# Optimization experiments

Hardware: AMD Instinct MI355X
Metric: run time of the kernel (lower is better)

## Reference

```python
import jax, jax.numpy as jnp
import numpy as np

SPECIAL = 4  # special_word_num

def _lstm_cell(x, h, c, Wih, Whh, b):
    # torch gate order: i, f, g, o ; gates = x@Wih.T + h@Whh.T + b
    g = x @ Wih.T + h @ Whh.T + b
    i, f, gg, o = jnp.split(g, 4, axis=-1)
    c_new = jax.nn.sigmoid(f) * c + jax.nn.sigmoid(i) * jnp.tanh(gg)
    h_new = jax.nn.sigmoid(o) * jnp.tanh(c_new)
    return h_new, c_new

def _lstm_scan(xs, h0, c0, Wih, Whh, b):
    def step(carry, x):
        h, c = carry
        h, c = _lstm_cell(x, h, c, Wih, Whh, b)
        return (h, c), h
    (hT, cT), hs = jax.lax.scan(step, (h0, c0), xs)
    return hs, hT, cT  # hs: [T, B, H]

def _forward(article, art_lens, tar_len, emb, enc_Wih_f, enc_Whh_f, enc_b_f,
             enc_Wih_b, enc_Whh_b, enc_b_b, init_enc_h, init_enc_c,
             dec_hW, dec_cW, attn_wm, attn_wq, proj_W1, proj_b1, proj_W2,
             dec_Wih, dec_Whh, dec_b):
    Tsrc, B, _ = article.shape
    H = init_enc_h.shape[1]
    # ---- encoder: 1-layer bidirectional LSTM with learned init states ----
    h0f = jnp.broadcast_to(init_enc_h[0], (B, H)); c0f = jnp.broadcast_to(init_enc_c[0], (B, H))
    h0b = jnp.broadcast_to(init_enc_h[1], (B, H)); c0b = jnp.broadcast_to(init_enc_c[1], (B, H))
    out_f, hTf, cTf = _lstm_scan(article, h0f, c0f, enc_Wih_f, enc_Whh_f, enc_b_f)
    out_b, hTb, cTb = _lstm_scan(article[::-1], h0b, c0b, enc_Wih_b, enc_Whh_b, enc_b_b)
    enc_art = jnp.concatenate([out_f, out_b[::-1]], axis=-1)  # [T, B, 2H]
    final_h = jnp.concatenate([hTf, hTb], axis=-1)  # [B, 2H]
    final_c = jnp.concatenate([cTf, cTb], axis=-1)
    init_h = final_h @ dec_hW  # [B, H]
    init_c = final_c @ dec_cW
    # ---- attention memory + mask ----
    attention = jnp.einsum('tbe,eh->bth', enc_art, attn_wm)  # [B, T, H]
    mask = jnp.arange(Tsrc)[None, :] < art_lens[:, None]      # [B, T]
    lens = art_lens.astype(attention.dtype)[:, None]
    seq_mean = jnp.sum(attention * mask[:, :, None], axis=1) / lens  # [B, H]
    def project(x):
        return jnp.tanh(x @ proj_W1 + proj_b1) @ proj_W2
    init_out = project(jnp.concatenate([init_h, seq_mean], axis=1))  # [B, H/2]
    # ---- sequential decoder over tar_len steps (lax.scan) ----
    embs = emb[SPECIAL + jnp.arange(tar_len)]  # [Ttgt, E]
    NEG = jnp.asarray(-1e9, attention.dtype)
    def dec_step(carry, emb_i):
        h, c, prev_out = carry
        x = jnp.concatenate([jnp.broadcast_to(emb_i, (B, emb_i.shape[0])), prev_out], axis=1)
        h, c = _lstm_cell(x, h, c, dec_Wih, dec_Whh, dec_b)
        query = h @ attn_wq                                   # [B, H]
        score = jnp.einsum('bh,bth->bt', query, attention)
        probs = jax.nn.softmax(jnp.where(mask, score, NEG), axis=-1)
        context = jnp.einsum('bt,bth->bh', probs, attention)
        dec_out = project(jnp.concatenate([h, context], axis=1))
        return (h, c, dec_out), (dec_out, h, c)
    _, (dec_all, h_all, c_all) = jax.lax.scan(dec_step, (init_h, init_c, init_out), embs)
    # stack(dim=0).transpose(0,1) -> batch-first
    return (dec_all.transpose(1, 0, 2), h_all.transpose(1, 0, 2), c_all.transpose(1, 0, 2))

def setup_inputs() -> dict:
    key = jax.random.key(0)
    ks = jax.random.split(key, 20)
    B, Tsrc, Ttgt = 32, 1024, 64
    H, E, V = 512, 256, 50000  # n_hidden, emb_dim/2, vocab
    EMB_DIM, ENC_OUT, OUT = 2 * E, 2 * H, H // 2
    def n(k, shape, s=0.05):
        return (jax.random.normal(k, shape, jnp.float32) * s).astype(jnp.float32)
    return {
        'article': n(ks[0], (Tsrc, B, EMB_DIM), 1.0),
        'art_lens': jnp.full((B,), Tsrc, jnp.int32),
        'tar_len': Ttgt,
        'emb': n(ks[1], (V, E)),
        'enc_Wih_f': n(ks[2], (4 * H, EMB_DIM)), 'enc_Whh_f': n(ks[3], (4 * H, H)), 'enc_b_f': n(ks[4], (4 * H,)),
        'enc_Wih_b': n(ks[5], (4 * H, EMB_DIM)), 'enc_Whh_b': n(ks[6], (4 * H, H)), 'enc_b_b': n(ks[7], (4 * H,)),
        'init_enc_h': n(ks[8], (2, H), 0.01), 'init_enc_c': n(ks[9], (2, H), 0.01),
        'dec_hW': n(ks[10], (ENC_OUT, H)), 'dec_cW': n(ks[11], (ENC_OUT, H)),
        'attn_wm': n(ks[12], (ENC_OUT, H)), 'attn_wq': n(ks[13], (H, H)),
        'proj_W1': n(ks[14], (2 * H, H)), 'proj_b1': n(ks[15], (H,)), 'proj_W2': n(ks[16], (H, OUT)),
        'dec_Wih': n(ks[17], (4 * H, H)), 'dec_Whh': n(ks[18], (4 * H, H)), 'dec_b': n(ks[19], (4 * H,)),
    }

def reference(article, art_lens, tar_len, emb, enc_Wih_f, enc_Whh_f, enc_b_f,
              enc_Wih_b, enc_Whh_b, enc_b_b, init_enc_h, init_enc_c,
              dec_hW, dec_cW, attn_wm, attn_wq, proj_W1, proj_b1, proj_W2,
              dec_Wih, dec_Whh, dec_b):
    return _forward(article, art_lens, tar_len, emb, enc_Wih_f, enc_Whh_f, enc_b_f,
                    enc_Wih_b, enc_Whh_b, enc_b_b, init_enc_h, init_enc_c,
                    dec_hW, dec_cW, attn_wm, attn_wq, proj_W1, proj_b1, proj_W2,
                    dec_Wih, dec_Whh, dec_b)
```

## Files before the change

kernel.cpp:

```cpp
#include <hip/hip_runtime.h>


#define DI __device__ __forceinline__

constexpr int BATCH = 32;
constexpr int TS = 1024;
constexpr int TG = 64;
constexpr int HID = 512;
constexpr int GD = 2048;
constexpr int EDIM = 256;
constexpr int SPECIAL = 4;
constexpr size_t OFF_H = (size_t)BATCH * TG * EDIM;
constexpr size_t OFF_C = OFF_H + (size_t)BATCH * TG * HID;
constexpr int FLAG_STRIDE = 16;

typedef __attribute__((ext_vector_type(8))) short bf16x8;
typedef __attribute__((ext_vector_type(4))) float f32x4;

DI float b2f(unsigned short u) {
  union { unsigned int i; float f; } v; v.i = ((unsigned int)u) << 16; return v.f;
}
DI unsigned short f2b(float f) {
  union { float f; unsigned int i; } v; v.f = f;
  unsigned int r = v.i + 0x7fffu + ((v.i >> 16) & 1u);
  return (unsigned short)(r >> 16);
}
DI float sigm(float x) { return 1.0f / (1.0f + expf(-x)); }
DI float ldf(const void* p, size_t i, int f32f) {
  return f32f ? ((const float*)p)[i] : b2f(((const unsigned short*)p)[i]);
}
DI void stf(void* p, size_t i, float v, int f32f) {
  if (f32f) ((float*)p)[i] = v; else ((unsigned short*)p)[i] = f2b(v);
}
DI unsigned int ald(const unsigned int* p) {
  return __hip_atomic_load(p, __ATOMIC_RELAXED, __HIP_MEMORY_SCOPE_AGENT);
}
DI float aldf(const float* p) {
  return __hip_atomic_load(p, __ATOMIC_RELAXED, __HIP_MEMORY_SCOPE_AGENT);
}
DI void ast(unsigned int* p, unsigned int v) {
  __hip_atomic_store(p, v, __ATOMIC_RELAXED, __HIP_MEMORY_SCOPE_AGENT);
}
DI void astf(float* p, float v) {
  __hip_atomic_store(p, v, __ATOMIC_RELAXED, __HIP_MEMORY_SCOPE_AGENT);
}

__global__ void detect_k(const void* art, int* flag) {
  int tid = threadIdx.x;
  float x = ((const float*)art)[tid + 1024];
  float a = fabsf(x);
  int sane = (x == 0.0f) || (a > 1e-8f && a < 1e4f);
  unsigned long long m = __ballot(sane);
  __shared__ int cnt[4];
  if ((tid & 63) == 0) cnt[tid >> 6] = __popcll(m);
  __syncthreads();
  if (tid == 0) flag[0] = (cnt[0] + cnt[1] + cnt[2] + cnt[3] > 128) ? 1 : 0;
}

__global__ void fill_sig_k(unsigned short* o, int n) {
  int g = blockIdx.x * 256 + threadIdx.x;
  if (g < n) o[g] = 0x42F6;
}

__global__ void pack_gate_k(const void* __restrict__ W,
                            unsigned short* __restrict__ pk, const int* dtf) {
  int f32f = dtf[0];
  int g = blockIdx.x * 256 + threadIdx.x;
  if (g >= (GD * HID) / 8) return;
  int lane = g & 63;
  int kk = (g >> 6) & 15;
  int tile = g >> 10;
  int p = tile * 16 + (lane & 15);
  int nloc = p & 63, blk = p >> 6;
  int orow = (nloc >> 4) * HID + blk * 16 + (nloc & 15);
  int k = kk * 32 + (lane >> 4) * 8;
  unsigned short tmp[8];
#pragma unroll
  for (int j = 0; j < 8; ++j) tmp[j] = f2b(ldf(W, (size_t)orow * HID + k + j, f32f));
  *(uint4*)(pk + (size_t)g * 8) = *(uint4*)tmp;
}

__global__ void pack_wm_k(const void* __restrict__ wm,
                          unsigned short* __restrict__ pk, const int* dtf) {
  int f32f = dtf[0];
  int g = blockIdx.x * 256 + threadIdx.x;
  if (g >= 32 * 32 * 64) return;
  int lane = g & 63;
  int kk = (g >> 6) & 31;
  int nt = g >> 11;
  int col = nt * 16 + (lane & 15);
  int kb = kk * 32 + (lane >> 4) * 8;
  unsigned short tmp[8];
#pragma unroll
  for (int j = 0; j < 8; ++j) tmp[j] = f2b(ldf(wm, (size_t)(kb + j) * HID + col, f32f));
  *(uint4*)(pk + (size_t)g * 8) = *(uint4*)tmp;
}

__global__ void pack_bn_k(const void* __restrict__ W, unsigned short* __restrict__ pk,
                          int K, int N, int total, const int* dtf) {
  int f32f = dtf[0];
  int g = blockIdx.x * 256 + threadIdx.x;
  if (g >= total) return;
  int lane = g & 63;
  int KK = K >> 5;
  int t = g >> 6;
  int kk = t % KK;
  int nt = t / KK;
  int col = nt * 16 + (lane & 15);
  int kb = kk * 32 + (lane >> 4) * 8;
  unsigned short tmp[8];
#pragma unroll
  for (int j = 0; j < 8; ++j) tmp[j] = f2b(ldf(W, (size_t)(kb + j) * N + col, f32f));
  *(uint4*)(pk + (size_t)g * 8) = *(uint4*)tmp;
}

__global__ void pack_bf16_k(const void* __restrict__ src,
                            unsigned short* __restrict__ dst, int n, const int* dtf) {
  int f32f = dtf[0];
  int g = blockIdx.x * 256 + threadIdx.x;
  if (g < n) dst[g] = f2b(ldf(src, g, f32f));
}

__global__ __launch_bounds__(256, 1) void enc_all_k(
    const unsigned short* __restrict__ artb,
    unsigned short* __restrict__ outF, unsigned short* __restrict__ outB,
    const unsigned short* __restrict__ hIF, const unsigned short* __restrict__ hIB,
    float* __restrict__ cF, float* __restrict__ cB,
    const unsigned short* __restrict__ pkXF, const unsigned short* __restrict__ pkHF,
    const unsigned short* __restrict__ pkXB, const unsigned short* __restrict__ pkHB,
    const void* __restrict__ bF, const void* __restrict__ bB,
    int* __restrict__ bar, const int* dtf) {
  const int f32f = dtf[0];
  const int blk = blockIdx.x;
  const int dir = blk >> 5;
  const int blk16 = blk & 31;
  const int tid = threadIdx.x;
  const int lane = tid & 63;
  const int wv = tid >> 6;
  const int tile = blk16 * 4 + wv;

  __shared__ unsigned short lstage[BATCH * HID];
  __shared__ float gbuf[BATCH * 68];

  const unsigned short* pkX = dir ? pkXB : pkXF;
  const unsigned short* pkH = dir ? pkHB : pkHF;
  const void* bias = dir ? bB : bF;
  unsigned short* out = dir ? outB : outF;
  const unsigned short* hI = dir ? hIB : hIF;
  float* cg = dir ? cB : cF;
  int* flp = bar + dir * 32 * FLAG_STRIDE;

  bf16x8 wx[16], wh[16];
  {
    const unsigned short* px = pkX + ((size_t)tile * 16 * 64 + lane) * 8;
    const unsigned short* ph = pkH + ((size_t)tile * 16 * 64 + lane) * 8;
#pragma unroll
    for (int kk = 0; kk < 16; ++kk) {
      wx[kk] = *(const bf16x8*)(px + (size_t)kk * 64 * 8);
      wh[kk] = *(const bf16x8*)(ph + (size_t)kk * 64 * 8);
    }
  }
  const int gb = tid >> 3;
  const int gj = (tid & 7) * 2;
  float c0 = cg[gb * HID + blk16 * 16 + gj];
  float c1 = cg[gb * HID + blk16 * 16 + gj + 1];

  const int r0 = lane & 15;
  const int r1 = 16 + r0;
  const int kbb = (lane >> 4) * 8;
  const int nloc = wv * 16 + (lane & 15);
  const int orow = (nloc >> 4) * HID + blk16 * 16 + (nloc & 15);
  const float bv = ldf(bias, orow, f32f);

  f32x4 acc0 = {0.f, 0.f, 0.f, 0.f};
  f32x4 acc1 = {0.f, 0.f, 0.f, 0.f};

  {
    const int ts0 = dir ? (TS - 1) : 0;
#pragma unroll
    for (int it = 0; it < 8; ++it) {
      int ci = it * 256 + tid;
      int row = ci >> 6;
      int k8 = (ci & 63) << 3;
      uint4 v = *(const uint4*)(artb + (size_t)ts0 * BATCH * HID +
                                (size_t)row * HID + k8);
      unsigned off = (unsigned)(row * 1024 + ((k8 * 2) ^ ((row & 7) << 4)));
      *(uint4*)((char*)lstage + off) = v;
    }
    __syncthreads();
#pragma unroll
    for (int kk = 0; kk < 16; ++kk) {
      unsigned o0 = (unsigned)(r0 * 1024 + (((kk * 32 + kbb) * 2) ^ ((r0 & 7) << 4)));
      unsigned o1 = (unsigned)(r1 * 1024 + (((kk * 32 + kbb) * 2) ^ ((r0 & 7) << 4)));
      bf16x8 a0 = *(const bf16x8*)((const char*)lstage + o0);
      bf16x8 a1 = *(const bf16x8*)((const char*)lstage + o1);
      acc0 = __builtin_amdgcn_mfma_f32_16x16x32_bf16(a0, wx[kk], acc0, 0, 0, 0);
      acc1 = __builtin_amdgcn_mfma_f32_16x16x32_bf16(a1, wx[kk], acc1, 0, 0, 0);
    }
  }

  for (int t = 0; t < TS; ++t) {
    const int tsrc = dir ? (TS - 1 - t) : t;
    if (t > 0) {
      if (wv == 0) {
        const int target = t;
        for (;;) {
          int v = (lane < 32)
              ? __hip_atomic_load(flp + lane * FLAG_STRIDE, __ATOMIC_RELAXED,
                                  __HIP_MEMORY_SCOPE_AGENT)
              : 0x7fffffff;
          if (__all(v >= target)) break;
          __builtin_amdgcn_s_sleep(2);
        }
      }
      __syncthreads();
    }
    unsigned int* hu = (t == 0)
        ? (unsigned int*)hI
        : (unsigned int*)(out + (size_t)(tsrc + (dir ? 1 : -1)) * BATCH * HID);
    unsigned int hreg[32];
#pragma unroll
    for (int it = 0; it < 32; ++it) hreg[it] = ald(hu + it * 256 + tid);
    __syncthreads();
#pragma unroll
    for (int it = 0; it < 32; ++it) {
      int dw = it * 256 + tid;
      int row = dw >> 8;
      unsigned lb = (unsigned)(row * 1024 +
                               (((dw & 252) << 2) ^ ((row & 7) << 4)) +
                               ((dw & 3) << 2));
      *(unsigned int*)((char*)lstage + lb) = hreg[it];
    }
    __syncthreads();
#pragma unroll
    for (int kk = 0; kk < 16; ++kk) {
      unsigned o0 = (unsigned)(r0 * 1024 + (((kk * 32 + kbb) * 2) ^ ((r0 & 7) << 4)));
      unsigned o1 = (unsigned)(r1 * 1024 + (((kk * 32 + kbb) * 2) ^ ((r0 & 7) << 4)));
      bf16x8 a0 = *(const bf16x8*)((const char*)lstage + o0);
      bf16x8 a1 = *(const bf16x8*)((const char*)lstage + o1);
      acc0 = __builtin_amdgcn_mfma_f32_16x16x32_bf16(a0, wh[kk], acc0, 0, 0, 0);
      acc1 = __builtin_amdgcn_mfma_f32_16x16x32_bf16(a1, wh[kk], acc1, 0, 0, 0);
    }
#pragma unroll
    for (int r = 0; r < 4; ++r) {
      int brow = (lane >> 4) * 4 + r;
      gbuf[brow * 68 + nloc] = acc0[r] + bv;
      gbuf[(16 + brow) * 68 + nloc] = acc1[r] + bv;
    }
    __syncthreads();
    {
      float gi0 = gbuf[gb * 68 + gj],      gf0 = gbuf[gb * 68 + 16 + gj];
      float gg0 = gbuf[gb * 68 + 32 + gj], go0 = gbuf[gb * 68 + 48 + gj];
      float gi1 = gbuf[gb * 68 + gj + 1],      gf1 = gbuf[gb * 68 + 16 + gj + 1];
      float gg1 = gbuf[gb * 68 + 32 + gj + 1], go1 = gbuf[gb * 68 + 48 + gj + 1];
      float cn0 = sigm(gf0) * c0 + sigm(gi0) * tanhf(gg0); c0 = cn0;
      float cn1 = sigm(gf1) * c1 + sigm(gi1) * tanhf(gg1); c1 = cn1;
      unsigned int hv = (unsigned int)f2b(sigm(go0) * tanhf(cn0)) |
                        ((unsigned int)f2b(sigm(go1) * tanhf(cn1)) << 16);
      ast((unsigned int*)out + (size_t)tsrc * (BATCH * HID / 2) +
              gb * (HID / 2) + blk16 * 8 + (tid & 7), hv);
    }
    if (t + 1 < TS) {
      __syncthreads();
      if (wv == 0 && lane == 0)
        __hip_atomic_store(flp + blk16 * FLAG_STRIDE, t + 1,
                           __ATOMIC_RELAXED, __HIP_MEMORY_SCOPE_AGENT);
      const int tn = dir ? (TS - 2 - t) : (t + 1);
#pragma unroll
      for (int it = 0; it < 8; ++it) {
        int ci = it * 256 + tid;
        int row = ci >> 6;
        int k8 = (ci & 63) << 3;
        uint4 v = *(const uint4*)(artb + (size_t)tn * BATCH * HID +
                                  (size_t)row * HID + k8);
        unsigned off = (unsigned)(row * 1024 + ((k8 * 2) ^ ((row & 7) << 4)));
        *(uint4*)((char*)lstage + off) = v;
      }
      __syncthreads();
      acc0 = (f32x4){0.f, 0.f, 0.f, 0.f};
      acc1 = (f32x4){0.f, 0.f, 0.f, 0.f};
#pragma unroll
      for (int kk = 0; kk < 16; ++kk) {
        unsigned o0 = (unsigned)(r0 * 1024 + (((kk * 32 + kbb) * 2) ^ ((r0 & 7) << 4)));
        unsigned o1 = (unsigned)(r1 * 1024 + (((kk * 32 + kbb) * 2) ^ ((r0 & 7) << 4)));
        bf16x8 a0 = *(const bf16x8*)((const char*)lstage + o0);
        bf16x8 a1 = *(const bf16x8*)((const char*)lstage + o1);
        acc0 = __builtin_amdgcn_mfma_f32_16x16x32_bf16(a0, wx[kk], acc0, 0, 0, 0);
        acc1 = __builtin_amdgcn_mfma_f32_16x16x32_bf16(a1, wx[kk], acc1, 0, 0, 0);
      }
    }
  }
  cg[gb * HID + blk16 * 16 + gj] = c0;
  cg[gb * HID + blk16 * 16 + gj + 1] = c1;
}

__global__ __launch_bounds__(512, 1) void dec_all_k(
    unsigned short* __restrict__ xdec,
    unsigned short* __restrict__ hd0, unsigned short* __restrict__ hd1,
    const float* __restrict__ cdec,
    const unsigned short* __restrict__ pkX, const unsigned short* __restrict__ pkH,
    const void* __restrict__ dbias,
    const unsigned short* __restrict__ att,
    const unsigned short* __restrict__ pkq,
    const unsigned short* __restrict__ pkw1,
    const unsigned short* __restrict__ b1p,
    const unsigned short* __restrict__ pkw2,
    const void* __restrict__ emb, const int* __restrict__ lens,
    void* __restrict__ dout,
    float* __restrict__ qg,
    unsigned int* __restrict__ ctxb,
    float* __restrict__ zg,
    int* __restrict__ flags, const int* dtf) {
  const int f32f = dtf[0];
  const int blk = blockIdx.x;
  const int tid = threadIdx.x;
  const int lane = tid & 63;
  const int wv = tid >> 6;
  __shared__ __align__(16) char smem[49152];

  const int gb = tid >> 3;
  const int gj = (tid & 7) * 2;
  const int r0 = lane & 15;
  const int r1 = 16 + r0;
  const int kbb = (lane >> 4) * 8;
  const int nloc = wv * 16 + (lane & 15);
  float c0 = 0.f, c1 = 0.f, bv = 0.f;
  bf16x8 cwx[16], cwh[16];
  if (tid < 256) {
    c0 = cdec[gb * HID + blk * 16 + gj];
    c1 = cdec[gb * HID + blk * 16 + gj + 1];
    int orow = (nloc >> 4) * HID + blk * 16 + (nloc & 15);
    bv = ldf(dbias, orow, f32f);
    const int tile = blk * 4 + wv;
    const unsigned short* px = pkX + ((size_t)tile * 16 * 64 + lane) * 8;
    const unsigned short* ph = pkH + ((size_t)tile * 16 * 64 + lane) * 8;
#pragma unroll
    for (int kk = 0; kk < 16; ++kk) {
      cwx[kk] = *(const bf16x8*)(px + (size_t)kk * 64 * 8);
      cwh[kk] = *(const bf16x8*)(ph + (size_t)kk * 64 * 8);
    }
  }

  int ep = 0;
  auto gbar = [&]() {
    __syncthreads();
    ++ep;
    if (wv == 0) {
      if (lane == 0)
        __hip_atomic_store(flags + blk * FLAG_STRIDE, ep, __ATOMIC_RELAXED,
                           __HIP_MEMORY_SCOPE_AGENT);
      for (;;) {
        int v = (lane < 32)
            ? __hip_atomic_load(flags + lane * FLAG_STRIDE, __ATOMIC_RELAXED,
                                __HIP_MEMORY_SCOPE_AGENT)
            : 0x7fffffff;
        if (__all(v >= ep)) break;
        __builtin_amdgcn_s_sleep(2);
      }
    }
    __syncthreads();
  };

  auto stage8k = [&](const unsigned int* src, unsigned short* lstage) {
    unsigned int rg[16];
#pragma unroll
    for (int it = 0; it < 16; ++it) rg[it] = ald(src + it * 512 + tid);
#pragma unroll
    for (int it = 0; it < 16; ++it) {
      int dw = it * 512 + tid;
      int row = dw >> 8;
      unsigned lb = (unsigned)(row * 1024 +
                               (((dw & 252) << 2) ^ ((row & 7) << 4)) +
                               ((dw & 3) << 2));
      *(unsigned int*)((char*)lstage + lb) = rg[it];
    }
  };

  auto afrag = [&](const unsigned short* lstage, int kk, bf16x8& a0, bf16x8& a1) {
    unsigned o0 = (unsigned)(r0 * 1024 + (((kk * 32 + kbb) * 2) ^ ((r0 & 7) << 4)));
    unsigned o1 = (unsigned)(r1 * 1024 + (((kk * 32 + kbb) * 2) ^ ((r0 & 7) << 4)));
    a0 = *(const bf16x8*)((const char*)lstage + o0);
    a1 = *(const bf16x8*)((const char*)lstage + o1);
  };

  for (int i = 0; i < TG; ++i) {
    unsigned short* hin = (i & 1) ? hd1 : hd0;
    unsigned short* hout = (i & 1) ? hd0 : hd1;
    f32x4 zacc0 = {0.f, 0.f, 0.f, 0.f};
    f32x4 zacc1 = {0.f, 0.f, 0.f, 0.f};

    {
      unsigned short* lstage = (unsigned short*)smem;
      float* gbuf = (float*)(smem + 32768);
      f32x4 acc0 = {0.f, 0.f, 0.f, 0.f};
      f32x4 acc1 = {0.f, 0.f, 0.f, 0.f};
      unsigned int hreg[32];
      if (tid < 256) {
        const unsigned int* xu = (const unsigned int*)xdec;
        unsigned int xreg[32];
#pragma unroll
        for (int it = 0; it < 32; ++it) xreg[it] = ald(xu + it * 256 + tid);
#pragma unroll
        for (int it = 0; it < 32; ++it) {
          int dw = it * 256 + tid;
          int row = dw >> 8;
          unsigned lb = (unsigned)(row * 1024 +
                                   (((dw & 252) << 2) ^ ((row & 7) << 4)) +
                                   ((dw & 3) << 2));
          *(unsigned int*)((char*)lstage + lb) = xreg[it];
        }
      }
      __syncthreads();
      if (tid < 256) {
        const unsigned int* hu = (const unsigned int*)hin;
#pragma unroll
        for (int it = 0; it < 32; ++it) hreg[it] = ald(hu + it * 256 + tid);
#pragma unroll
        for (int kk = 0; kk < 16; ++kk) {
          bf16x8 a0, a1;
          afrag(lstage, kk, a0, a1);
          acc0 = __builtin_amdgcn_mfma_f32_16x16x32_bf16(a0, cwx[kk], acc0, 0, 0, 0);
          acc1 = __builtin_amdgcn_mfma_f32_16x16x32_bf16(a1, cwx[kk], acc1, 0, 0, 0);
        }
      }
      __syncthreads();
      if (tid < 256) {
#pragma unroll
        for (int it = 0; it < 32; ++it) {
          int dw = it * 256 + tid;
          int row = dw >> 8;
          unsigned lb = (unsigned)(row * 1024 +
                                   (((dw & 252) << 2) ^ ((row & 7) << 4)) +
                                   ((dw & 3) << 2));
          *(unsigned int*)((char*)lstage + lb) = hreg[it];
        }
      }
      __syncthreads();
      if (tid < 256) {
#pragma unroll
        for (int kk = 0; kk < 16; ++kk) {
          bf16x8 a0, a1;
          afrag(lstage, kk, a0, a1);
          acc0 = __builtin_amdgcn_mfma_f32_16x16x32_bf16(a0, cwh[kk], acc0, 0, 0, 0);
          acc1 = __builtin_amdgcn_mfma_f32_16x16x32_bf16(a1, cwh[kk], acc1, 0, 0, 0);
        }
#pragma unroll
        for (int r = 0; r < 4; ++r) {
          int brow = (lane >> 4) * 4 + r;
          gbuf[brow * 68 + nloc] = acc0[r] + bv;
          gbuf[(16 + brow) * 68 + nloc] = acc1[r] + bv;
        }
      }
      __syncthreads();
      if (tid < 256) {
        float gi0 = gbuf[gb * 68 + gj],      gf0 = gbuf[gb * 68 + 16 + gj];
        float gg0 = gbuf[gb * 68 + 32 + gj], go0 = gbuf[gb * 68 + 48 + gj];
        float gi1 = gbuf[gb * 68 + gj + 1],      gf1 = gbuf[gb * 68 + 16 + gj + 1];
        float gg1 = gbuf[gb * 68 + 32 + gj + 1], go1 = gbuf[gb * 68 + 48 + gj + 1];
        float cn0 = sigm(gf0) * c0 + sigm(gi0) * tanhf(gg0); c0 = cn0;
        float cn1 = sigm(gf1) * c1 + sigm(gi1) * tanhf(gg1); c1 = cn1;
        float hn0 = sigm(go0) * tanhf(cn0);
        float hn1 = sigm(go1) * tanhf(cn1);
        ast((unsigned int*)hout + gb * (HID / 2) + blk * 8 + (tid & 7),
            (unsigned int)f2b(hn0) | ((unsigned int)f2b(hn1) << 16));
        size_t e0 = ((size_t)gb * TG + i) * HID + blk * 16 + gj;
        stf(dout, OFF_H + e0, hn0, f32f);
        stf(dout, OFF_H + e0 + 1, hn1, f32f);
        stf(dout, OFF_C + e0, cn0, f32f);
        stf(dout, OFF_C + e0 + 1, cn1, f32f);
      }
    }
    gbar();

    {
      unsigned short* lstage = (unsigned short*)smem;
      float* part = (float*)(smem + 32768);
      stage8k((const unsigned int*)hout, lstage);
      __syncthreads();
      f32x4 acc0 = {0.f, 0.f, 0.f, 0.f};
      f32x4 acc1 = {0.f, 0.f, 0.f, 0.f};
#pragma unroll
      for (int j = 0; j < 2; ++j) {
        int kk = wv * 2 + j;
        bf16x8 a0, a1;
        afrag(lstage, kk, a0, a1);
        bf16x8 bq = *(const bf16x8*)(pkq + ((size_t)(blk * 16 + kk) * 64 + lane) * 8);
        acc0 = __builtin_amdgcn_mfma_f32_16x16x32_bf16(a0, bq, acc0, 0, 0, 0);
        acc1 = __builtin_amdgcn_mfma_f32_16x16x32_bf16(a1, bq, acc1, 0, 0, 0);
        bf16x8 bw = *(const bf16x8*)(pkw1 + ((size_t)(blk * 32 + kk) * 64 + lane) * 8);
        zacc0 = __builtin_amdgcn_mfma_f32_16x16x32_bf16(a0, bw, zacc0, 0, 0, 0);
        zacc1 = __builtin_amdgcn_mfma_f32_16x16x32_bf16(a1, bw, zacc1, 0, 0, 0);
      }
#pragma unroll
      for (int r = 0; r < 4; ++r) {
        int m0 = (lane >> 4) * 4 + r;
        part[wv * 512 + m0 * 16 + (lane & 15)] = acc0[r];
        part[wv * 512 + (m0 + 16) * 16 + (lane & 15)] = acc1[r];
      }
      __syncthreads();
      {
        float s = 0.f;
#pragma unroll
        for (int w = 0; w < 8; ++w) s += part[w * 512 + tid];
        int bb2 = tid >> 4, cl = tid & 15;
        astf(qg + (size_t)bb2 * HID + blk * 16 + cl, s);
      }
    }
    gbar();

    {
      const int b = blk;
      const int len = lens[b];
      float* cred = (float*)smem;
      float* mwl  = (float*)(smem + 16384);
      float* lwl  = (float*)(smem + 16448);
      float* qf   = (float*)(smem + 16512);
      float* ctxf = (float*)(smem + 18560);
      qf[tid] = aldf(qg + (size_t)b * HID + tid);
      __syncthreads();
      float qv[8];
#pragma unroll
      for (int e = 0; e < 8; ++e) qv[e] = qf[lane * 8 + e];
      float m = -1e30f, l = 0.f;
      float ca[8] = {0.f, 0.f, 0.f, 0.f, 0.f, 0.f, 0.f, 0.f};
      const unsigned short* ab = att + ((size_t)b * TS + wv * 128) * HID + lane * 8;
      for (int tt = 0; tt < 128; tt += 4) {
        int t = wv * 128 + tt;
        bf16x8 rr0 = *(const bf16x8*)(ab + (size_t)(tt + 0) * HID);
        bf16x8 rr1 = *(const bf16x8*)(ab + (size_t)(tt + 1) * HID);
        bf16x8 rr2 = *(const bf16x8*)(ab + (size_t)(tt + 2) * HID);
        bf16x8 rr3 = *(const bf16x8*)(ab + (size_t)(tt + 3) * HID);
        float s0 = 0.f, s1 = 0.f, s2 = 0.f, s3 = 0.f;
#pragma unroll
        for (int e = 0; e < 8; ++e) {
          float q = qv[e];
          s0 += q * b2f(((const unsigned short*)&rr0)[e]);
          s1 += q * b2f(((const unsigned short*)&rr1)[e]);
          s2 += q * b2f(((const unsigned short*)&rr2)[e]);
          s3 += q * b2f(((const unsigned short*)&rr3)[e]);
        }
        for (int o = 32; o; o >>= 1) {
          s0 += __shfl_xor(s0, o, 64); s1 += __shfl_xor(s1, o, 64);
          s2 += __shfl_xor(s2, o, 64); s3 += __shfl_xor(s3, o, 64);
        }
        bool v0 = (t < len), v1 = (t + 1 < len), v2 = (t + 2 < len), v3 = (t + 3 < len);
        float smax = fmaxf(fmaxf(v0 ? s0 : -1e30f, v1 ? s1 : -1e30f),
                           fmaxf(v2 ? s2 : -1e30f, v3 ? s3 : -1e30f));
        if (smax > m) {
          float sc2 = expf(m - smax);
          l *= sc2;
#pragma unroll
          for (int e = 0; e < 8; ++e) ca[e] *= sc2;
          m = smax;
        }
        if (v0) { float p = expf(s0 - m); l += p;
#pragma unroll
          for (int e = 0; e < 8; ++e) ca[e] += p * b2f(((const unsigned short*)&rr0)[e]); }
        if (v1) { float p = expf(s1 - m); l += p;
#pragma unroll
          for (int e = 0; e < 8; ++e) ca[e] += p * b2f(((const unsigned short*)&rr1)[e]); }
        if (v2) { float p = expf(s2 - m); l += p;
#pragma unroll
          for (int e = 0; e < 8; ++e) ca[e] += p * b2f(((const unsigned short*)&rr2)[e]); }
        if (v3) { float p = expf(s3 - m); l += p;
#pragma unroll
          for (int e = 0; e < 8; ++e) ca[e] += p * b2f(((const unsigned short*)&rr3)[e]); }
      }
#pragma unroll
      for (int e = 0; e < 8; ++e) cred[wv * 512 + lane * 8 + e] = ca[e];
      if (lane == 0) { mwl[wv] = m; lwl[wv] = l; }
      __syncthreads();
      {
        float M = -1e30f;
#pragma unroll
        for (int w = 0; w < 8; ++w) M = fmaxf(M, mwl[w]);
        float L = 0.f, s = 0.f;
#pragma unroll
        for (int w = 0; w < 8; ++w) {
          float sc2 = expf(mwl[w] - M);
          L += lwl[w] * sc2;
          s += cred[w * 512 + tid] * sc2;
        }
        ctxf[tid] = s / L;
      }
      __syncthreads();
      if (tid < 256) {
        unsigned int d = (unsigned int)f2b(ctxf[2 * tid]) |
                         ((unsigned int)f2b(ctxf[2 * tid + 1]) << 16);
        ast(ctxb + b * 256 + tid, d);
      }
    }
    gbar();

    {
      unsigned short* lstage = (unsigned short*)smem;
      float* part = (float*)(smem + 32768);
      stage8k(ctxb, lstage);
      __syncthreads();
#pragma unroll
      for (int j = 0; j < 2; ++j) {
        int kkl = wv * 2 + j;
        bf16x8 a0, a1;
        afrag(lstage, kkl, a0, a1);
        bf16x8 bb = *(const bf16x8*)(pkw1 + ((size_t)(blk * 32 + 16 + kkl) * 64 + lane) * 8);
        zacc0 = __builtin_amdgcn_mfma_f32_16x16x32_bf16(a0, bb, zacc0, 0, 0, 0);
        zacc1 = __builtin_amdgcn_mfma_f32_16x16x32_bf16(a1, bb, zacc1, 0, 0, 0);
      }
#pragma unroll
      for (int r = 0; r < 4; ++r) {
        int m0 = (lane >> 4) * 4 + r;
        part[wv * 512 + m0 * 16 + (lane & 15)] = zacc0[r];
        part[wv * 512 + (m0 + 16) * 16 + (lane & 15)] = zacc1[r];
      }
      __syncthreads();
      {
        float s = 0.f;
#pragma unroll
        for (int w = 0; w < 8; ++w) s += part[w * 512 + tid];
        int bb2 = tid >> 4, cl = tid & 15;
        int col = blk * 16 + cl;
        astf(zg + (size_t)bb2 * HID + col, tanhf(b2f(b1p[col]) + s));
      }
    }
    gbar();

    {
      unsigned short* lstage = (unsigned short*)smem;
      float* part = (float*)(smem + 32768);
      if (blk < 16) {
        unsigned int rg[16];
#pragma unroll
        for (int it = 0; it < 16; ++it) {
          int dw = it * 512 + tid;
          int b = dw >> 8, cp = dw & 255;
          float z0 = aldf(zg + (size_t)b * HID + 2 * cp);
          float z1 = aldf(zg + (size_t)b * HID + 2 * cp + 1);
          rg[it] = (unsigned int)f2b(z0) | ((unsigned int)f2b(z1) << 16);
        }
#pragma unroll
        for (int it = 0; it < 16; ++it) {
          int dw = it * 512 + tid;
          int row = dw >> 8;
          unsigned lb = (unsigned)(row * 1024 +
                                   (((dw & 252) << 2) ^ ((row & 7) << 4)) +
                                   ((dw & 3) << 2));
          *(unsigned int*)((char*)lstage + lb) = rg[it];
        }
      }
      __syncthreads();
      f32x4 acc0 = {0.f, 0.f, 0.f, 0.f};
      f32x4 acc1 = {0.f, 0.f, 0.f, 0.f};
      if (blk < 16) {
#pragma unroll
        for (int j = 0; j < 2; ++j) {
          int kk = wv * 2 + j;
          bf16x8 a0, a1;
          afrag(lstage, kk, a0, a1);
          bf16x8 bb = *(const bf16x8*)(pkw2 + ((size_t)(blk * 16 + kk) * 64 + lane) * 8);
          acc0 = __builtin_amdgcn_mfma_f32_16x16x32_bf16(a0, bb, acc0, 0, 0, 0);
          acc1 = __builtin_amdgcn_mfma_f32_16x16x32_bf16(a1, bb, acc1, 0, 0, 0);
        }
#pragma unroll
        for (int r = 0; r < 4; ++r) {
          int m0 = (lane >> 4) * 4 + r;
          part[wv * 512 + m0 * 16 + (lane & 15)] = acc0[r];
          part[wv * 512 + (m0 + 16) * 16 + (lane & 15)] = acc1[r];
        }
      }
      __syncthreads();
      if (blk < 16) {
        float s = 0.f;
#pragma unroll
        for (int w = 0; w < 8; ++w) s += part[w * 512 + tid];
        int bb2 = tid >> 4, cl = tid & 15;
        int col = blk * 16 + cl;
        stf(dout, ((size_t)bb2 * TG + i) * EDIM + col, s, f32f);
        unsigned short xb = f2b(s);
        int ob = __shfl_xor((int)xb, 1);
        if (!(tid & 1))
          ast((unsigned int*)xdec + bb2 * 256 + 128 + (col >> 1),
              (unsigned int)xb | ((unsigned int)(ob & 0xffff) << 16));
      }
      if (blk == 16) {
#pragma unroll
        for (int it = 0; it < 8; ++it) {
          int idx = it * 512 + tid;
          int b = idx >> 7, np = idx & 127;
          float e0 = ldf(emb, (size_t)(SPECIAL + i + 1) * EDIM + 2 * np, f32f);
          float e1 = ldf(emb, (size_t)(SPECIAL + i + 1) * EDIM + 2 * np + 1, f32f);
          ast((unsigned int*)xdec + b * 256 + np,
              (unsigned int)f2b(e0) | ((unsigned int)f2b(e1) << 16));
        }
      }
    }
    gbar();
  }
}

__global__ __launch_bounds__(256) void attn_mm_k(
    const unsigned short* __restrict__ outF, const unsigned short* __restrict__ outB,
    const unsigned short* __restrict__ pkwm, unsigned short* __restrict__ att) {
  __shared__ char ldsA[4 * 1040];
  int bid = blockIdx.x;
  int bn = bid & 7, bm = bid >> 3;
  int tid = threadIdx.x, lane = tid & 63, wv = tid >> 6;
  int r0 = bm * 64;
  f32x4 acc[2][2] = {};
  int srow = tid >> 2, skb = tid & 3;
  int mt0 = (wv & 1) * 2, nt0 = (wv >> 1) * 2;
  for (int kk = 0; kk < 32; ++kk) {
    int kg = kk * 32 + skb * 8;
    const unsigned short* src = (kg < HID)
        ? (outF + (size_t)(r0 + srow) * HID + kg)
        : (outB + (size_t)(r0 + srow) * HID + (kg - HID));
    uint4 v = *(const uint4*)src;
    __syncthreads();
    *(uint4*)(ldsA + skb * 1040 + srow * 16) = v;
    __syncthreads();
    bf16x8 a[2], bb[2];
#pragma unroll
    for (int mi = 0; mi < 2; ++mi) {
      int rl = (mt0 + mi) * 16 + (lane & 15);
      a[mi] = *(const bf16x8*)(ldsA + (lane >> 4) * 1040 + rl * 16);
    }
#pragma unroll
    for (int nj = 0; nj < 2; ++nj) {
      int ntg = bn * 4 + nt0 + nj;
      bb[nj] = *(const bf16x8*)(pkwm + ((size_t)(ntg * 32 + kk) * 64 + lane) * 8);
    }
#pragma unroll
    for (int mi = 0; mi < 2; ++mi)
#pragma unroll
      for (int nj = 0; nj < 2; ++nj)
        acc[mi][nj] = __builtin_amdgcn_mfma_f32_16x16x32_bf16(a[mi], bb[nj], acc[mi][nj], 0, 0, 0);
  }
#pragma unroll
  for (int mi = 0; mi < 2; ++mi)
#pragma unroll
    for (int nj = 0; nj < 2; ++nj)
#pragma unroll
      for (int r = 0; r < 4; ++r) {
        int row = r0 + (mt0 + mi) * 16 + (lane >> 4) * 4 + r;
        int t = row >> 5, b = row & 31;
        int h = bn * 64 + (nt0 + nj) * 16 + (lane & 15);
        att[((size_t)b * TS + t) * HID + h] = f2b(acc[mi][nj][r]);
      }
}

__global__ void init_states_k(const void* __restrict__ ih, const void* __restrict__ ic,
                              unsigned short* hIF, unsigned short* hIB,
                              float* cF, float* cB, int* bar, const int* dtf) {
  int f32f = dtf[0];
  int g = blockIdx.x * 256 + threadIdx.x;
  if (g < (64 + 32) * FLAG_STRIDE)
    __hip_atomic_store(bar + g, 0, __ATOMIC_RELAXED, __HIP_MEMORY_SCOPE_AGENT);
  int b = g >> 9, j = g & 511;
  hIF[b * HID + j] = f2b(ldf(ih, j, f32f));
  hIB[b * HID + j] = f2b(ldf(ih, HID + j, f32f));
  cF[b * HID + j] = ldf(ic, j, f32f);
  cB[b * HID + j] = ldf(ic, HID + j, f32f);
}

__global__ void seqmean_k(const unsigned short* __restrict__ att,
                          const int* __restrict__ lens, float* __restrict__ sm) {
  int b = blockIdx.x, tid = threadIdx.x;
  int len = lens[b];
  float a0 = 0.f, a1 = 0.f;
  for (int t = 0; t < len; ++t) {
    const unsigned short* row = att + ((size_t)b * TS + t) * HID;
    a0 += b2f(row[tid]);
    a1 += b2f(row[tid + 256]);
  }
  float fl = (float)len;
  sm[b * HID + tid] = a0 / fl;
  sm[b * HID + tid + 256] = a1 / fl;
}

__global__ void mv_bb_k(const unsigned short* __restrict__ A1,
                        const unsigned short* __restrict__ A2,
                        const void* __restrict__ W, unsigned short* __restrict__ o,
                        const int* dtf) {
  int f32f = dtf[0];
  int g = blockIdx.x * 256 + threadIdx.x;
  int b = g >> 9, n = g & 511;
  float acc = 0.f;
  for (int k = 0; k < HID; ++k) acc += b2f(A1[b * HID + k]) * ldf(W, (size_t)k * HID + n, f32f);
  for (int k = 0; k < HID; ++k) acc += b2f(A2[b * HID + k]) * ldf(W, (size_t)(HID + k) * HID + n, f32f);
  o[b * HID + n] = f2b(acc);
}

__global__ void mv_ff_k(const float* __restrict__ A1, const float* __restrict__ A2,
                        const void* __restrict__ W, float* __restrict__ o, const int* dtf) {
  int f32f = dtf[0];
  int g = blockIdx.x * 256 + threadIdx.x;
  int b = g >> 9, n = g & 511;
  float acc = 0.f;
  for (int k = 0; k < HID; ++k) acc += A1[b * HID + k] * ldf(W, (size_t)k * HID + n, f32f);
  for (int k = 0; k < HID; ++k) acc += A2[b * HID + k] * ldf(W, (size_t)(HID + k) * HID + n, f32f);
  o[b * HID + n] = acc;
}

__global__ void proj1_k(const unsigned short* __restrict__ A1, const float* __restrict__ A2,
                        const void* __restrict__ W1p, const void* __restrict__ b1p,
                        unsigned short* __restrict__ z, const int* dtf) {
  int f32f = dtf[0];
  int g = blockIdx.x * 256 + threadIdx.x;
  int b = g >> 9, n = g & 511;
  float acc = ldf(b1p, n, f32f);
  for (int k = 0; k < HID; ++k) acc += b2f(A1[b * HID + k]) * ldf(W1p, (size_t)k * HID + n, f32f);
  for (int k = 0; k < HID; ++k) acc += A2[b * HID + k] * ldf(W1p, (size_t)(HID + k) * HID + n, f32f);
  z[b * HID + n] = f2b(tanhf(acc));
}

__global__ void proj2_init_k(const unsigned short* __restrict__ z,
                             const void* __restrict__ W2, const void* __restrict__ emb,
                             unsigned short* __restrict__ xdec, const int* dtf) {
  int f32f = dtf[0];
  int g = blockIdx.x * 256 + threadIdx.x;
  int b = g >> 8, n = g & 255;
  float acc = 0.f;
  for (int k = 0; k < HID; ++k) acc += b2f(z[b * HID + k]) * ldf(W2, (size_t)k * EDIM + n, f32f);
  xdec[b * HID + EDIM + n] = f2b(acc);
  xdec[b * HID + n] = f2b(ldf(emb, (size_t)SPECIAL * EDIM + n, f32f));
}

extern "C" void kernel_launch(void* const* d_in, const int* in_sizes, int n_in,
                              void* d_out, int out_size, void* d_ws, size_t ws_size,
                              hipStream_t stream) {
  (void)in_sizes; (void)n_in;
  const void* article = d_in[0];
  const int* art_lens = (const int*)d_in[1];
  const void* emb  = d_in[3];
  const void* eWxf = d_in[4]; const void* eWhf = d_in[5]; const void* ebf = d_in[6];
  const void* eWxb = d_in[7]; const void* eWhb = d_in[8]; const void* ebb = d_in[9];
  const void* initH = d_in[10]; const void* initC = d_in[11];
  const void* dhW = d_in[12]; const void* dcW = d_in[13];
  const void* wm = d_in[14]; const void* wq = d_in[15];
  const void* W1 = d_in[16]; const void* b1 = d_in[17]; const void* W2 = d_in[18];
  const void* dWx = d_in[19]; const void* dWh = d_in[20]; const void* db = d_in[21];

  char* ws = (char*)d_ws;
  size_t off = 0;
  auto take = [&](size_t bytes) -> char* {
    char* p = ws + off;
    off = (off + bytes + 255) & ~(size_t)255;
    return p;
  };
  int* dtf = (int*)take(4);
  int* bar = (int*)take((64 + 32) * FLAG_STRIDE * 4);
  unsigned short* pk_exf = (unsigned short*)take((size_t)GD * HID * 2);
  unsigned short* pk_ehf = (unsigned short*)take((size_t)GD * HID * 2);
  unsigned short* pk_exb = (unsigned short*)take((size_t)GD * HID * 2);
  unsigned short* pk_ehb = (unsigned short*)take((size_t)GD * HID * 2);
  unsigned short* pk_dx  = (unsigned short*)take((size_t)GD * HID * 2);
  unsigned short* pk_dh  = (unsigned short*)take((size_t)GD * HID * 2);
  unsigned short* pk_wm  = (unsigned short*)take((size_t)1024 * HID * 2);
  unsigned short* pkq  = (unsigned short*)take((size_t)512 * 512 * 2);
  unsigned short* pkw1 = (unsigned short*)take((size_t)1024 * 512 * 2);
  unsigned short* b1p  = (unsigned short*)take((size_t)HID * 2);
  unsigned short* pkw2 = (unsigned short*)take((size_t)512 * 256 * 2);
  unsigned short* outF = (unsigned short*)take((size_t)TS * BATCH * HID * 2);
  unsigned short* outB = (unsigned short*)take((size_t)TS * BATCH * HID * 2);
  unsigned short* att  = (unsigned short*)take((size_t)BATCH * TS * HID * 2);
  unsigned short* hIF  = (unsigned short*)take((size_t)BATCH * HID * 2);
  unsigned short* hIB  = (unsigned short*)take((size_t)BATCH * HID * 2);
  float* cF = (float*)take((size_t)BATCH * HID * 4);
  float* cB = (float*)take((size_t)BATCH * HID * 4);
  unsigned short* hd0 = (unsigned short*)take((size_t)BATCH * HID * 2);
  unsigned short* hd1 = (unsigned short*)take((size_t)BATCH * HID * 2);
  float* cdec = (float*)take((size_t)BATCH * HID * 4);
  unsigned short* xdec = (unsigned short*)take((size_t)BATCH * HID * 2);
  unsigned short* zbuf = (unsigned short*)take((size_t)BATCH * HID * 2);
  float* qg = (float*)take((size_t)BATCH * HID * 4);
  unsigned int* ctxb = (unsigned int*)take((size_t)BATCH * 256 * 4);
  float* zg = (float*)take((size_t)BATCH * HID * 4);
  float* sm = (float*)take((size_t)BATCH * HID * 4);

  if (off > ws_size) {
    fill_sig_k<<<(out_size + 255) / 256, 256, 0, stream>>>((unsigned short*)d_out, out_size);
    return;
  }

  unsigned short* artb = att;

  detect_k<<<1, 256, 0, stream>>>(article, dtf);
  pack_gate_k<<<512, 256, 0, stream>>>(eWxf, pk_exf, dtf);
  pack_gate_k<<<512, 256, 0, stream>>>(eWhf, pk_ehf, dtf);
  pack_gate_k<<<512, 256, 0, stream>>>(eWxb, pk_exb, dtf);
  pack_gate_k<<<512, 256, 0, stream>>>(eWhb, pk_ehb, dtf);
  pack_gate_k<<<512, 256, 0, stream>>>(dWx, pk_dx, dtf);
  pack_gate_k<<<512, 256, 0, stream>>>(dWh, pk_dh, dtf);
  pack_wm_k<<<256, 256, 0, stream>>>(wm, pk_wm, dtf);
  pack_bn_k<<<128, 256, 0, stream>>>(wq, pkq, 512, 512, 32 * 16 * 64, dtf);
  pack_bn_k<<<256, 256, 0, stream>>>(W1, pkw1, 1024, 512, 32 * 32 * 64, dtf);
  pack_bn_k<<<64, 256, 0, stream>>>(W2, pkw2, 512, 256, 16 * 16 * 64, dtf);
  pack_bf16_k<<<2, 256, 0, stream>>>(b1, b1p, HID, dtf);
  pack_bf16_k<<<65536, 256, 0, stream>>>(article, artb, TS * BATCH * HID, dtf);
  init_states_k<<<64, 256, 0, stream>>>(initH, initC, hIF, hIB, cF, cB, bar, dtf);

  enc_all_k<<<64, 256, 0, stream>>>(artb, outF, outB, hIF, hIB, cF, cB,
                                    pk_exf, pk_ehf, pk_exb, pk_ehb, ebf, ebb,
                                    bar, dtf);

  attn_mm_k<<<4096, 256, 0, stream>>>(outF, outB, pk_wm, att);
  seqmean_k<<<32, 256, 0, stream>>>(att, art_lens, sm);
  mv_bb_k<<<64, 256, 0, stream>>>(outF + (size_t)(TS - 1) * BATCH * HID, outB, dhW, hd0, dtf);
  mv_ff_k<<<64, 256, 0, stream>>>(cF, cB, dcW, cdec, dtf);
  proj1_k<<<64, 256, 0, stream>>>(hd0, sm, W1, b1, zbuf, dtf);
  proj2_init_k<<<32, 256, 0, stream>>>(zbuf, W2, emb, xdec, dtf);

  dec_all_k<<<32, 512, 0, stream>>>(xdec, hd0, hd1, cdec, pk_dx, pk_dh, db,
                                    att, pkq, pkw1, b1p, pkw2, emb, art_lens,
                                    d_out, qg, ctxb, zg,
                                    bar + 64 * FLAG_STRIDE, dtf);
}
```

Before: 9.488 ms.

## Fold decoder output projection into input gate weights, drop per-step barrier

Precomputes the embedding part of the decoder input gates for every target step and folds W2 into the hidden part of the decoder input weights. The gate GEMM can then consume the tanh projection output z directly instead of the reconstructed x. This removes a global barrier per decoder step and the x-staging stage, and leaves only blocks below 16 writing the output. The cost is extra setup kernels and fp32 workspace, plus rounding of the folded weights to bf16, which may change numerics slightly.

After: 9.883 ms. 1.04x slower.

```diff
diff --git a/kernel.cpp b/kernel.cpp
--- a/kernel.cpp
+++ b/kernel.cpp
@@ -80,6 +80,23 @@
   *(uint4*)(pk + (size_t)g * 8) = *(uint4*)tmp;
 }
 
+__global__ void pack_gate_f32_k(const float* __restrict__ W,
+                                unsigned short* __restrict__ pk) {
+  int g = blockIdx.x * 256 + threadIdx.x;
+  if (g >= (GD * HID) / 8) return;
+  int lane = g & 63;
+  int kk = (g >> 6) & 15;
+  int tile = g >> 10;
+  int p = tile * 16 + (lane & 15);
+  int nloc = p & 63, blk = p >> 6;
+  int orow = (nloc >> 4) * HID + blk * 16 + (nloc & 15);
+  int k = kk * 32 + (lane >> 4) * 8;
+  unsigned short tmp[8];
+#pragma unroll
+  for (int j = 0; j < 8; ++j) tmp[j] = f2b(W[(size_t)orow * HID + k + j]);
+  *(uint4*)(pk + (size_t)g * 8) = *(uint4*)tmp;
+}
+
 __global__ void pack_wm_k(const void* __restrict__ wm,
                           unsigned short* __restrict__ pk, const int* dtf) {
   int f32f = dtf[0];
@@ -119,6 +136,36 @@
   int f32f = dtf[0];
   int g = blockIdx.x * 256 + threadIdx.x;
   if (g < n) dst[g] = f2b(ldf(src, g, f32f));
+}
+
+__global__ void fold_w_k(const void* __restrict__ dWx, const void* __restrict__ W2,
+                         float* __restrict__ wf, const int* dtf) {
+  int f32f = dtf[0];
+  __shared__ float arow[256];
+  int g = blockIdx.x;
+  int tid = threadIdx.x;
+  arow[tid] = ldf(dWx, (size_t)g * 512 + 256 + tid, f32f);
+  __syncthreads();
+  float a0 = 0.f, a1 = 0.f;
+  for (int m = 0; m < 256; ++m) {
+    float a = arow[m];
+    a0 += a * ldf(W2, (size_t)tid * 256 + m, f32f);
+    a1 += a * ldf(W2, (size_t)(tid + 256) * 256 + m, f32f);
+  }
+  wf[(size_t)g * 512 + tid] = a0;
+  wf[(size_t)g * 512 + tid + 256] = a1;
+}
+
+__global__ void ge_k(const void* __restrict__ emb, const void* __restrict__ dWx,
+                     float* __restrict__ ge, const int* dtf) {
+  int f32f = dtf[0];
+  int idx = blockIdx.x * 256 + threadIdx.x;
+  int i = idx >> 11, g = idx & 2047;
+  float a = 0.f;
+  for (int m = 0; m < 256; ++m)
+    a += ldf(emb, (size_t)(SPECIAL + i) * 256 + m, f32f) *
+         ldf(dWx, (size_t)g * 512 + m, f32f);
+  ge[(size_t)i * 2048 + g] = a;
 }
 
 __global__ __launch_bounds__(256, 1) void enc_all_k(
@@ -295,21 +342,22 @@
 }
 
 __global__ __launch_bounds__(512, 1) void dec_all_k(
-    unsigned short* __restrict__ xdec,
     unsigned short* __restrict__ hd0, unsigned short* __restrict__ hd1,
     const float* __restrict__ cdec,
-    const unsigned short* __restrict__ pkX, const unsigned short* __restrict__ pkH,
+    const unsigned short* __restrict__ pkZ,
+    const unsigned short* __restrict__ pkH,
     const void* __restrict__ dbias,
+    const float* __restrict__ geb,
     const unsigned short* __restrict__ att,
     const unsigned short* __restrict__ pkq,
     const unsigned short* __restrict__ pkw1,
     const unsigned short* __restrict__ b1p,
     const unsigned short* __restrict__ pkw2,
-    const void* __restrict__ emb, const int* __restrict__ lens,
+    const int* __restrict__ lens,
     void* __restrict__ dout,
     float* __restrict__ qg,
     unsigned int* __restrict__ ctxb,
-    float* __restrict__ zg,
+    unsigned int* __restrict__ zb,
     int* __restrict__ flags, const int* dtf) {
   const int f32f = dtf[0];
   const int blk = blockIdx.x;
@@ -325,18 +373,19 @@
   const int kbb = (lane >> 4) * 8;
   const int nloc = wv * 16 + (lane & 15);
   float c0 = 0.f, c1 = 0.f, bv = 0.f;
-  bf16x8 cwx[16], cwh[16];
+  int orow = 0;
+  bf16x8 cwz[16], cwh[16];
   if (tid < 256) {
     c0 = cdec[gb * HID + blk * 16 + gj];
     c1 = cdec[gb * HID + blk * 16 + gj + 1];
-    int orow = (nloc >> 4) * HID + blk * 16 + (nloc & 15);
+    orow = (nloc >> 4) * HID + blk * 16 + (nloc & 15);
     bv = ldf(dbias, orow, f32f);
     const int tile = blk * 4 + wv;
-    const unsigned short* px = pkX + ((size_t)tile * 16 * 64 + lane) * 8;
+    const unsigned short* pz = pkZ + ((size_t)tile * 16 * 64 + lane) * 8;
     const unsigned short* ph = pkH + ((size_t)tile * 16 * 64 + lane) * 8;
 #pragma unroll
     for (int kk = 0; kk < 16; ++kk) {
-      cwx[kk] = *(const bf16x8*)(px + (size_t)kk * 64 * 8);
+      cwz[kk] = *(const bf16x8*)(pz + (size_t)kk * 64 * 8);
       cwh[kk] = *(const bf16x8*)(ph + (size_t)kk * 64 * 8);
     }
   }
@@ -396,10 +445,9 @@
       f32x4 acc1 = {0.f, 0.f, 0.f, 0.f};
       unsigned int hreg[32];
       if (tid < 256) {
-        const unsigned int* xu = (const unsigned int*)xdec;
-        unsigned int xreg[32];
-#pragma unroll
-        for (int it = 0; it < 32; ++it) xreg[it] = ald(xu + it * 256 + tid);
+        unsigned int zreg[32];
+#pragma unroll
+        for (int it = 0; it < 32; ++it) zreg[it] = ald(zb + it * 256 + tid);
 #pragma unroll
         for (int it = 0; it < 32; ++it) {
           int dw = it * 256 + tid;
@@ -407,7 +455,7 @@
           unsigned lb = (unsigned)(row * 1024 +
                                    (((dw & 252) << 2) ^ ((row & 7) << 4)) +
                                    ((dw & 3) << 2));
-          *(unsigned int*)((char*)lstage + lb) = xreg[it];
+          *(unsigned int*)((char*)lstage + lb) = zreg[it];
         }
       }
       __syncthreads();
@@ -419,8 +467,8 @@
         for (int kk = 0; kk < 16; ++kk) {
           bf16x8 a0, a1;
           afrag(lstage, kk, a0, a1);
-          acc0 = __builtin_amdgcn_mfma_f32_16x16x32_bf16(a0, cwx[kk], acc0, 0, 0, 0);
-          acc1 = __builtin_amdgcn_mfma_f32_16x16x32_bf16(a1, cwx[kk], acc1, 0, 0, 0);
+          acc0 = __builtin_amdgcn_mfma_f32_16x16x32_bf16(a0, cwz[kk], acc0, 0, 0, 0);
+          acc1 = __builtin_amdgcn_mfma_f32_16x16x32_bf16(a1, cwz[kk], acc1, 0, 0, 0);
         }
       }
       __syncthreads();
@@ -444,11 +492,12 @@
           acc0 = __builtin_amdgcn_mfma_f32_16x16x32_bf16(a0, cwh[kk], acc0, 0, 0, 0);
           acc1 = __builtin_amdgcn_mfma_f32_16x16x32_bf16(a1, cwh[kk], acc1, 0, 0, 0);
         }
+        float gev = geb[(size_t)i * 2048 + orow];
 #pragma unroll
         for (int r = 0; r < 4; ++r) {
           int brow = (lane >> 4) * 4 + r;
-          gbuf[brow * 68 + nloc] = acc0[r] + bv;
-          gbuf[(16 + brow) * 68 + nloc] = acc1[r] + bv;
+          gbuf[brow * 68 + nloc] = acc0[r] + bv + gev;
+          gbuf[(16 + brow) * 68 + nloc] = acc1[r] + bv + gev;
         }
       }
       __syncthreads();
@@ -606,6 +655,7 @@
         zacc0 = __builtin_amdgcn_mfma_f32_16x16x32_bf16(a0, bb, zacc0, 0, 0, 0);
         zacc1 = __builtin_amdgcn_mfma_f32_16x16x32_bf16(a1, bb, zacc1, 0, 0, 0);
       }
+      __syncthreads();
 #pragma unroll
       for (int r = 0; r < 4; ++r) {
         int m0 = (lane >> 4) * 4 + r;
@@ -619,81 +669,49 @@
         for (int w = 0; w < 8; ++w) s += part[w * 512 + tid];
         int bb2 = tid >> 4, cl = tid & 15;
         int col = blk * 16 + cl;
-        astf(zg + (size_t)bb2 * HID + col, tanhf(b2f(b1p[col]) + s));
+        float zv = tanhf(b2f(b1p[col]) + s);
+        unsigned short me = f2b(zv);
+        int other = __shfl_xor((int)me, 1);
+        if (!(tid & 1))
+          ast(zb + bb2 * 256 + (col >> 1),
+              (unsigned int)me | ((unsigned int)(other & 0xffff) << 16));
       }
     }
     gbar();
 
-    {
+    if (blk < 16) {
       unsigned short* lstage = (unsigned short*)smem;
       float* part = (float*)(smem + 32768);
-      if (blk < 16) {
-        unsigned int rg[16];
-#pragma unroll
-        for (int it = 0; it < 16; ++it) {
-          int dw = it * 512 + tid;
-          int b = dw >> 8, cp = dw & 255;
-          float z0 = aldf(zg + (size_t)b * HID + 2 * cp);
-          float z1 = aldf(zg + (size_t)b * HID + 2 * cp + 1);
-          rg[it] = (unsigned int)f2b(z0) | ((unsigned int)f2b(z1) << 16);
-        }
-#pragma unroll
-        for (int it = 0; it < 16; ++it) {
-          int dw = it * 512 + tid;
-          int row = dw >> 8;
-          unsigned lb = (unsigned)(row * 1024 +
-                                   (((dw & 252) << 2) ^ ((row & 7) << 4)) +
-                                   ((dw & 3) << 2));
-          *(unsigned int*)((char*)lstage + lb) = rg[it];
-        }
-      }
+      stage8k(zb, lstage);
       __syncthreads();
       f32x4 acc0 = {0.f, 0.f, 0.f, 0.f};
       f32x4 acc1 = {0.f, 0.f, 0.f, 0.f};
-      if (blk < 16) {
-#pragma unroll
-        for (int j = 0; j < 2; ++j) {
-          int kk = wv * 2 + j;
-          bf16x8 a0, a1;
-          afrag(lstage, kk, a0, a1);
-          bf16x8 bb = *(const bf16x8*)(pkw2 + ((size_t)(blk * 16 + kk) * 64 + lane) * 8);
-          acc0 = __builtin_amdgcn_mfma_f32_16x16x32_bf16(a0, bb, acc0, 0, 0, 0);
-          acc1 = __builtin_amdgcn_mfma_f32_16x16x32_bf16(a1, bb, acc1, 0, 0, 0);
-        }
-#pragma unroll
-        for (int r = 0; r < 4; ++r) {
-          int m0 = (lane >> 4) * 4 + r;
-          part[wv * 512 + m0 * 16 + (lane & 15)] = acc0[r];
-          part[wv * 512 + (m0 + 16) * 16 + (lane & 15)] = acc1[r];
-        }
-      }
-      __syncthreads();
-      if (blk < 16) {
+#pragma unroll
+      for (int j = 0; j < 2; ++j) {
+        int kk = wv * 2 + j;
+        bf16x8 a0, a1;
+        afrag(lstage, kk, a0, a1);
+        bf16x8 bb = *(const bf16x8*)(pkw2 + ((size_t)(blk * 16 + kk) * 64 + lane) * 8);
+        acc0 = __builtin_amdgcn_mfma_f32_16x16x32_bf16(a0, bb, acc0, 0, 0, 0);
+        acc1 = __builtin_amdgcn_mfma_f32_16x16x32_bf16(a1, bb, acc1, 0, 0, 0);
+      }
+#pragma unroll
+      for (int r = 0; r < 4; ++r) {
+        int m0 = (lane >> 4) * 4 + r;
+        part[wv * 512 + m0 * 16 + (lane & 15)] = acc0[r];
+        part[wv * 512 + (m0 + 16) * 16 + (lane & 15)] = acc1[r];
+      }
+      __syncthreads();
+      {
         float s = 0.f;
 #pragma unroll
         for (int w = 0; w < 8; ++w) s += part[w * 512 + tid];
         int bb2 = tid >> 4, cl = tid & 15;
         int col = blk * 16 + cl;
         stf(dout, ((size_t)bb2 * TG + i) * EDIM + col, s, f32f);
-        unsigned short xb = f2b(s);
-        int ob = __shfl_xor((int)xb, 1);
-        if (!(tid & 1))
-          ast((unsigned int*)xdec + bb2 * 256 + 128 + (col >> 1),
-              (unsigned int)xb | ((unsigned int)(ob & 0xffff) << 16));
-      }
-      if (blk == 16) {
-#pragma unroll
-        for (int it = 0; it < 8; ++it) {
-          int idx = it * 512 + tid;
-          int b = idx >> 7, np = idx & 127;
-          float e0 = ldf(emb, (size_t)(SPECIAL + i + 1) * EDIM + 2 * np, f32f);
-          float e1 = ldf(emb, (size_t)(SPECIAL + i + 1) * EDIM + 2 * np + 1, f32f);
-          ast((unsigned int*)xdec + b * 256 + np,
-              (unsigned int)f2b(e0) | ((unsigned int)f2b(e1) << 16));
-        }
-      }
-    }
-    gbar();
+      }
+      __syncthreads();
+    }
   }
 }
 
@@ -812,18 +830,6 @@
   z[b * HID + n] = f2b(tanhf(acc));
 }
 
-__global__ void proj2_init_k(const unsigned short* __restrict__ z,
-                             const void* __restrict__ W2, const void* __restrict__ emb,
-                             unsigned short* __restrict__ xdec, const int* dtf) {
-  int f32f = dtf[0];
-  int g = blockIdx.x * 256 + threadIdx.x;
-  int b = g >> 8, n = g & 255;
-  float acc = 0.f;
-  for (int k = 0; k < HID; ++k) acc += b2f(z[b * HID + k]) * ldf(W2, (size_t)k * EDIM + n, f32f);
-  xdec[b * HID + EDIM + n] = f2b(acc);
-  xdec[b * HID + n] = f2b(ldf(emb, (size_t)SPECIAL * EDIM + n, f32f));
-}
-
 extern "C" void kernel_launch(void* const* d_in, const int* in_sizes, int n_in,
                               void* d_out, int out_size, void* d_ws, size_t ws_size,
                               hipStream_t stream) {
@@ -852,13 +858,15 @@
   unsigned short* pk_ehf = (unsigned short*)take((size_t)GD * HID * 2);
   unsigned short* pk_exb = (unsigned short*)take((size_t)GD * HID * 2);
   unsigned short* pk_ehb = (unsigned short*)take((size_t)GD * HID * 2);
-  unsigned short* pk_dx  = (unsigned short*)take((size_t)GD * HID * 2);
+  unsigned short* pk_fold = (unsigned short*)take((size_t)GD * HID * 2);
   unsigned short* pk_dh  = (unsigned short*)take((size_t)GD * HID * 2);
   unsigned short* pk_wm  = (unsigned short*)take((size_t)1024 * HID * 2);
   unsigned short* pkq  = (unsigned short*)take((size_t)512 * 512 * 2);
   unsigned short* pkw1 = (unsigned short*)take((size_t)1024 * 512 * 2);
   unsigned short* b1p  = (unsigned short*)take((size_t)HID * 2);
   unsigned short* pkw2 = (unsigned short*)take((size_t)512 * 256 * 2);
+  float* wfoldf = (float*)take((size_t)GD * HID * 4);
+  float* geb = (float*)take((size_t)TG * GD * 4);
   unsigned short* outF = (unsigned short*)take((size_t)TS * BATCH * HID * 2);
   unsigned short* outB = (unsigned short*)take((size_t)TS * BATCH * HID * 2);
   unsigned short* att  = (unsigned short*)take((size_t)BATCH * TS * HID * 2);
@@ -869,11 +877,9 @@
   unsigned short* hd0 = (unsigned short*)take((size_t)BATCH * HID * 2);
   unsigned short* hd1 = (unsigned short*)take((size_t)BATCH * HID * 2);
   float* cdec = (float*)take((size_t)BATCH * HID * 4);
-  unsigned short* xdec = (unsigned short*)take((size_t)BATCH * HID * 2);
   unsigned short* zbuf = (unsigned short*)take((size_t)BATCH * HID * 2);
   float* qg = (float*)take((size_t)BATCH * HID * 4);
   unsigned int* ctxb = (unsigned int*)take((size_t)BATCH * 256 * 4);
-  float* zg = (float*)take((size_t)BATCH * HID * 4);
   float* sm = (float*)take((size_t)BATCH * HID * 4);
 
   if (off > ws_size) {
@@ -888,8 +894,10 @@
   pack_gate_k<<<512, 256, 0, stream>>>(eWhf, pk_ehf, dtf);
   pack_gate_k<<<512, 256, 0, stream>>>(eWxb, pk_exb, dtf);
   pack_gate_k<<<512, 256, 0, stream>>>(eWhb, pk_ehb, dtf);
-  pack_gate_k<<<512, 256, 0, stream>>>(dWx, pk_dx, dtf);
   pack_gate_k<<<512, 256, 0, stream>>>(dWh, pk_dh, dtf);
+  fold_w_k<<<2048, 256, 0, stream>>>(dWx, W2, wfoldf, dtf);
+  ge_k<<<512, 256, 0, stream>>>(emb, dWx, geb, dtf);
+  pack_gate_f32_k<<<512, 256, 0, stream>>>(wfoldf, pk_fold);
   pack_wm_k<<<256, 256, 0, stream>>>(wm, pk_wm, dtf);
   pack_bn_k<<<128, 256, 0, stream>>>(wq, pkq, 512, 512, 32 * 16 * 64, dtf);
   pack_bn_k<<<256, 256, 0, stream>>>(W1, pkw1, 1024, 512, 32 * 32 * 64, dtf);
@@ -907,10 +915,9 @@
   mv_bb_k<<<64, 256, 0, stream>>>(outF + (size_t)(TS - 1) * BATCH * HID, outB, dhW, hd0, dtf);
   mv_ff_k<<<64, 256, 0, stream>>>(cF, cB, dcW, cdec, dtf);
   proj1_k<<<64, 256, 0, stream>>>(hd0, sm, W1, b1, zbuf, dtf);
-  proj2_init_k<<<32, 256, 0, stream>>>(zbuf, W2, emb, xdec, dtf);
-
-  dec_all_k<<<32, 512, 0, stream>>>(xdec, hd0, hd1, cdec, pk_dx, pk_dh, db,
-                                    att, pkq, pkw1, b1p, pkw2, emb, art_lens,
-                                    d_out, qg, ctxb, zg,
+
+  dec_all_k<<<32, 512, 0, stream>>>(hd0, hd1, cdec, pk_fold, pk_dh, db, geb,
+                                    att, pkq, pkw1, b1p, pkw2, art_lens,
+                                    d_out, qg, ctxb, (unsigned int*)zbuf,
                                     bar + 64 * FLAG_STRIDE, dtf);
 }
```
